# Kernel optimization log

Hardware: AMD Instinct MI355X
Metric: run time of the kernel (lower is better)

The kernel has to match this reference:

```python
import jax, jax.numpy as jnp
import numpy as np
from jax import lax

DIM = 256
HEADS = 8
SR = 4
EPS = 1e-5
SCALE = (DIM // HEADS) ** -0.5


def _dwconv(x, wgt, stride, pad):
    # x: (B,C,H,W), wgt: (C,1,kh,kw) depthwise
    return lax.conv_general_dilated(
        x, wgt, (stride, stride), [(pad, pad), (pad, pad)],
        feature_group_count=x.shape[1],
        dimension_numbers=("NCHW", "OIHW", "NCHW"))


def _bn(x, g, b, m, v):
    # eval-mode batchnorm folded to per-channel scale/shift
    s = g / jnp.sqrt(v + EPS)
    return x * s[:, None, None] + (b - m * s)[:, None, None]


def setup_inputs() -> dict:
    key = jax.random.key(0)
    ks = jax.random.split(key, 16)
    b, h, w = 8, 64, 64
    c = DIM
    n = h * w

    def rn(k, shape, s=0.05):
        return jax.random.normal(k, shape, jnp.float32) * s

    return dict(
        x=jax.random.normal(ks[0], (b, n, c), jnp.float32),
        h=h, w=w,
        Wq=rn(ks[1], (c, c)), bq=rn(ks[2], (c,)),
        Wkv=rn(ks[3], (2 * c, c)), bkv=rn(ks[4], (2 * c,)),
        sr_w1=rn(ks[5], (c, 1, SR + 3, SR + 3), 0.1),
        bn1_gamma=1.0 + rn(ks[6], (c,)), bn1_beta=rn(ks[7], (c,)),
        bn1_mean=rn(ks[8], (c,)), bn1_var=jnp.abs(1.0 + rn(ks[9], (c,))),
        sr_w2=1.0 + rn(ks[10], (c,), 0.2),  # 1x1 depthwise conv == per-channel scale
        bn2_gamma=1.0 + rn(ks[11], (c,)), bn2_beta=rn(ks[12], (c,)),
        bn2_mean=rn(ks[13], (c,)), bn2_var=jnp.abs(1.0 + rn(ks[14], (c,))),
        local_w=rn(ks[15], (c, 1, 3, 3), 0.1),
        local_b=jnp.zeros((c,), jnp.float32),
    )


def reference(x, h, w, Wq, bq, Wkv, bkv, sr_w1, bn1_gamma, bn1_beta, bn1_mean,
              bn1_var, sr_w2, bn2_gamma, bn2_beta, bn2_mean, bn2_var,
              local_w, local_b):
    b, n, c = x.shape
    hd = c // HEADS
    xi = x.transpose(0, 2, 1).reshape(b, c, h, w)  # (b,c,h,w)

    # q projection (1x1 conv == channel matmul)
    q = jnp.einsum("bchw,dc->bdhw", xi, Wq) + bq[None, :, None, None]
    q = q.reshape(b, HEADS, hd, n).transpose(0, 1, 3, 2)  # (b,H,n,hd)

    # spatial reduction: dwconv7 s4 + BN + GELU + dw1x1 + BN
    kv = _dwconv(xi, sr_w1, SR, (SR + 3) // 2)
    kv = _bn(kv, bn1_gamma, bn1_beta, bn1_mean, bn1_var)
    kv = jax.nn.gelu(kv, approximate=False)
    kv = kv * sr_w2[None, :, None, None]
    kv = _bn(kv, bn2_gamma, bn2_beta, bn2_mean, bn2_var)

    # residual local depthwise 3x3 conv
    kv = _dwconv(kv, local_w, 1, 1) + local_b[None, :, None, None] + kv

    # kv projection and split
    kvp = jnp.einsum("bchw,dc->bdhw", kv, Wkv) + bkv[None, :, None, None]
    k_, v_ = jnp.split(kvp, 2, axis=1)
    m = k_.shape[2] * k_.shape[3]
    k_ = k_.reshape(b, HEADS, hd, m)                       # (b,H,hd,m)
    v_ = v_.reshape(b, HEADS, hd, m).transpose(0, 1, 3, 2)  # (b,H,m,hd)

    attn = jax.nn.softmax(jnp.einsum("bhnd,bhdm->bhnm", q, k_) * SCALE, axis=-1)
    out = jnp.einsum("bhnm,bhmd->bhnd", attn, v_)           # (b,H,n,hd)
    out = out.transpose(0, 1, 3, 2).reshape(b, c, n).transpose(0, 2, 1)
    return out
```

## Files before the change

### kernel.cpp

```cpp
#include <hip/hip_runtime.h>
#include <math.h>

typedef __bf16 bf16;
typedef bf16 bf16x4 __attribute__((ext_vector_type(4)));
typedef bf16 bf16x8 __attribute__((ext_vector_type(8)));
typedef float f32x4 __attribute__((ext_vector_type(4)));

static_assert(sizeof(bf16x8) == 16, "bf16x8 must be 16B");

#define QSCALE (0.17677669529663687f * 1.4426950408889634f)

__device__ __forceinline__ f32x4 mfma16(bf16x8 a, bf16x8 b, f32x4 c) {
  return __builtin_amdgcn_mfma_f32_16x16x32_bf16(a, b, c, 0, 0, 0);
}

__global__ __launch_bounds__(256) void k_cvt(
    const float* __restrict__ Wq, const float* __restrict__ Wkv,
    const float* __restrict__ w7, bf16* __restrict__ Wqb,
    bf16* __restrict__ Wkvb, float* __restrict__ w7t) {
  const int tid = threadIdx.x;
  const int blk = blockIdx.x;
  if (blk < 96) {
    const float* src;
    bf16* dst;
    if (blk < 32) {
      const int idx = blk * 256 + tid;
      src = Wq + (size_t)idx * 8;
      dst = Wqb + (size_t)idx * 8;
    } else {
      const int idx = (blk - 32) * 256 + tid;
      src = Wkv + (size_t)idx * 8;
      dst = Wkvb + (size_t)idx * 8;
    }
    const float4 a = ((const float4*)src)[0];
    const float4 b = ((const float4*)src)[1];
    bf16x8 r;
    r[0] = (bf16)a.x; r[1] = (bf16)a.y; r[2] = (bf16)a.z; r[3] = (bf16)a.w;
    r[4] = (bf16)b.x; r[5] = (bf16)b.y; r[6] = (bf16)b.z; r[7] = (bf16)b.w;
    *(bf16x8*)dst = r;
  } else {
    const int c = tid;
    #pragma unroll
    for (int tap = 0; tap < 49; tap++)
      w7t[tap * 256 + c] = w7[c * 49 + tap];
  }
}

__global__ __launch_bounds__(256, 2) void k_sr(
    const float* __restrict__ x, const float* __restrict__ w7t,
    const float* __restrict__ g1, const float* __restrict__ b1,
    const float* __restrict__ m1, const float* __restrict__ v1,
    const float* __restrict__ sw2,
    const float* __restrict__ g2, const float* __restrict__ b2,
    const float* __restrict__ m2, const float* __restrict__ v2,
    bf16* __restrict__ kv1) {
  __shared__ float part[4][256];
  const int tid = threadIdx.x;
  const int team = tid >> 6, g = tid & 63;
  const int c0 = g * 4;
  const int blk = blockIdx.x;
  const int b = blk & 7, m = blk >> 3;
  const int oy = m >> 4, ox = m & 15;

  float4 xv[13], wv[13];
  float msk[13];
  #pragma unroll
  for (int j = 0; j < 13; j++) {
    const int tap = team + j * 4;
    const int ky = tap / 7, kx = tap - ky * 7;
    const int iy = oy * 4 - 3 + ky, ix = ox * 4 - 3 + kx;
    msk[j] = (tap < 49 && iy >= 0 && iy < 64 && ix >= 0 && ix < 64) ? 1.f : 0.f;
    const int iyc = iy < 0 ? 0 : (iy > 63 ? 63 : iy);
    const int ixc = ix < 0 ? 0 : (ix > 63 ? 63 : ix);
    const int tc = tap > 48 ? 48 : tap;
    xv[j] = *(const float4*)(x + ((size_t)b * 4096 + iyc * 64 + ixc) * 256 + c0);
    wv[j] = *(const float4*)(w7t + tc * 256 + c0);
  }
  float a0 = 0.f, a1 = 0.f, a2 = 0.f, a3 = 0.f;
  #pragma unroll
  for (int j = 0; j < 13; j++) {
    a0 += xv[j].x * wv[j].x * msk[j];
    a1 += xv[j].y * wv[j].y * msk[j];
    a2 += xv[j].z * wv[j].z * msk[j];
    a3 += xv[j].w * wv[j].w * msk[j];
  }
  *(f32x4*)&part[team][c0] = (f32x4){a0, a1, a2, a3};
  __syncthreads();
  const int c = tid;
  float y = part[0][c] + part[1][c] + part[2][c] + part[3][c];
  float s = g1[c] / sqrtf(v1[c] + 1e-5f);
  y = y * s + (b1[c] - m1[c] * s);
  y = 0.5f * y * (1.f + erff(y * 0.70710678118654752f));
  y *= sw2[c];
  s = g2[c] / sqrtf(v2[c] + 1e-5f);
  y = y * s + (b2[c] - m2[c] * s);
  kv1[((size_t)b * 256 + m) * 256 + c] = (bf16)y;
}

__global__ __launch_bounds__(256) void k_localkv(
    const bf16* __restrict__ kv1, const float* __restrict__ w3,
    const float* __restrict__ lb, const bf16* __restrict__ Wkvb,
    const float* __restrict__ bkv, bf16* __restrict__ k_a,
    bf16* __restrict__ v_b) {
  __shared__ bf16 halo[3][10][256];
  __shared__ float rows[8][256];
  const int c = threadIdx.x;
  const int mt = blockIdx.x;
  const int part = blockIdx.y;
  const int b = blockIdx.z;
  const int oy = mt >> 1, o0 = (mt & 1) * 8;

  #pragma unroll
  for (int p = 0; p < 30; p++) {
    const int dy = p / 10, xi = p - dy * 10;
    const int iy = oy - 1 + dy, ix = o0 - 1 + xi;
    const bool ok = (iy >= 0 && iy < 16 && ix >= 0 && ix < 16);
    const int iyc = ok ? iy : 0, ixc = ok ? ix : 0;
    const bf16 v = kv1[((size_t)b * 256 + iyc * 16 + ixc) * 256 + c];
    halo[dy][xi][c] = ok ? v : (bf16)0.f;
  }
  float w3f[9];
  #pragma unroll
  for (int t = 0; t < 9; t++) w3f[t] = w3[c * 9 + t];
  const float lbf = lb[c];
  __syncthreads();

  #pragma unroll
  for (int r = 0; r < 8; r++) {
    float acc = lbf + (float)halo[1][r + 1][c];
    #pragma unroll
    for (int ky = 0; ky < 3; ky++)
      #pragma unroll
      for (int kx = 0; kx < 3; kx++)
        acc += (float)halo[ky][r + kx][c] * w3f[ky * 3 + kx];
    rows[r][c] = acc;
  }
  __syncthreads();

  const int tid = c;
  const size_t wrow = (size_t)tid + (part ? 256 : 0);
  float accs[8] = {0};
  for (int oc = 0; oc < 32; oc++) {
    const bf16x8 w0 = *(const bf16x8*)(Wkvb + wrow * 256 + oc * 8);
    float wf0[8];
    #pragma unroll
    for (int j = 0; j < 8; j++) wf0[j] = (float)w0[j];
    #pragma unroll
    for (int r = 0; r < 8; r++) {
      const float4* rp = (const float4*)&rows[r][oc * 8];
      const float4 ra = rp[0], rb = rp[1];
      const float rv[8] = {ra.x, ra.y, ra.z, ra.w, rb.x, rb.y, rb.z, rb.w};
      #pragma unroll
      for (int j = 0; j < 8; j++) accs[r] += wf0[j] * rv[j];
    }
  }
  const float bias = bkv[wrow];
  const int h = tid >> 5, d = tid & 31;
  if (part == 0) {
    #pragma unroll
    for (int r = 0; r < 8; r++) {
      const int m = (oy * 16 + o0) + r;
      k_a[(((size_t)b * 8 + h) * 256 + m) * 32 + d] = (bf16)(accs[r] + bias);
    }
  } else {
    #pragma unroll
    for (int r = 0; r < 8; r++) {
      const int m = (oy * 16 + o0) + r;
      v_b[(((size_t)b * 8 + h) * 32 + d) * 256 + m] = (bf16)(accs[r] + bias);
    }
  }
}

__global__ __launch_bounds__(256) void k_qproj(
    const float* __restrict__ x, const bf16* __restrict__ Wqb,
    const float* __restrict__ bq, bf16* __restrict__ q_ws) {
  __shared__ bf16 xs[32 * 264];
  const int tid = threadIdx.x, wv = tid >> 6, lane = tid & 63;
  const int qd = lane >> 4, l15 = lane & 15;
  const size_t rowbase = (size_t)blockIdx.x * 32;

  #pragma unroll
  for (int it = 0; it < 4; it++) {
    const int idx = it * 256 + tid;
    const int lr = idx >> 5, pos = idx & 31;
    const float* src = x + (rowbase + lr) * 256 + pos * 8;
    const float4 a = ((const float4*)src)[0];
    const float4 b = ((const float4*)src)[1];
    bf16x8 r;
    r[0] = (bf16)a.x; r[1] = (bf16)a.y; r[2] = (bf16)a.z; r[3] = (bf16)a.w;
    r[4] = (bf16)b.x; r[5] = (bf16)b.y; r[6] = (bf16)b.z; r[7] = (bf16)b.w;
    *(bf16x8*)(xs + lr * 264 + pos * 8) = r;
  }
  __syncthreads();

  f32x4 acc0[4], acc1[4];
  #pragma unroll
  for (int dt = 0; dt < 4; dt++) {
    acc0[dt] = (f32x4){0.f, 0.f, 0.f, 0.f};
    acc1[dt] = (f32x4){0.f, 0.f, 0.f, 0.f};
  }
  #pragma unroll 2
  for (int kc = 0; kc < 8; kc++) {
    const bf16x8 a0 = *(const bf16x8*)(xs + l15 * 264 + kc * 32 + qd * 8);
    const bf16x8 a1 = *(const bf16x8*)(xs + (16 + l15) * 264 + kc * 32 + qd * 8);
    #pragma unroll
    for (int dt = 0; dt < 4; dt++) {
      const int d = wv * 64 + dt * 16 + l15;
      const bf16x8 bb = *(const bf16x8*)(Wqb + (size_t)d * 256 + kc * 32 + qd * 8);
      acc0[dt] = mfma16(a0, bb, acc0[dt]);
      acc1[dt] = mfma16(a1, bb, acc1[dt]);
    }
  }
  #pragma unroll
  for (int dt = 0; dt < 4; dt++) {
    const int d = wv * 64 + dt * 16 + l15;
    const float bias = bq[d];
    const int h = d >> 5, dl = d & 31;
    #pragma unroll
    for (int r = 0; r < 4; r++) {
      const size_t row0 = rowbase + qd * 4 + r;
      const size_t row1 = rowbase + 16 + qd * 4 + r;
      q_ws[(((row0 >> 12) * 8 + h) * 4096 + (row0 & 4095)) * 32 + dl] =
          (bf16)((acc0[dt][r] + bias) * QSCALE);
      q_ws[(((row1 >> 12) * 8 + h) * 4096 + (row1 & 4095)) * 32 + dl] =
          (bf16)((acc1[dt][r] + bias) * QSCALE);
    }
  }
}

__global__ __launch_bounds__(256) void k_attn(
    const bf16* __restrict__ q_ws, const bf16* __restrict__ k_a,
    const bf16* __restrict__ v_b, float* __restrict__ out) {
  __shared__ float comb[2][36][64];
  const int tid = threadIdx.x;
  const int wv = tid >> 6, lane = tid & 63;
  const int pair = wv >> 1, half = wv & 1;
  const int qd = lane >> 4, l15 = lane & 15;
  const int b = blockIdx.z, h = blockIdx.y;
  const int bh = b * 8 + h;
  const int n_base = blockIdx.x * 128 + pair * 64;

  const bf16* qb = q_ws + ((size_t)bh * 4096 + n_base) * 32;
  bf16x8 qf[4];
  #pragma unroll
  for (int qi = 0; qi < 4; qi++)
    qf[qi] = *(const bf16x8*)(qb + (size_t)(qi * 16 + l15) * 32 + qd * 8);

  const bf16* kb = k_a + ((size_t)bh * 256 + half * 128) * 32;
  const bf16* vb = v_b + (size_t)bh * 32 * 256 + half * 128;

  f32x4 acc[4][2];
  float lr[4] = {0.f, 0.f, 0.f, 0.f};
  #pragma unroll
  for (int qi = 0; qi < 4; qi++) {
    acc[qi][0] = (f32x4){0.f, 0.f, 0.f, 0.f};
    acc[qi][1] = (f32x4){0.f, 0.f, 0.f, 0.f};
  }
  const int kperm = 8 * (l15 >> 2) + (l15 & 3);

  bf16x8 ka0 = *(const bf16x8*)(kb + (size_t)kperm * 32 + qd * 8);
  bf16x8 ka1 = *(const bf16x8*)(kb + (size_t)(kperm + 4) * 32 + qd * 8);
  bf16x8 va0 = *(const bf16x8*)(vb + (size_t)l15 * 256 + qd * 8);
  bf16x8 va1 = *(const bf16x8*)(vb + (size_t)(16 + l15) * 256 + qd * 8);

  for (int ch = 0; ch < 4; ch++) {
    const int cn = (ch < 3 ? ch + 1 : 3) * 32;
    const bf16x8 nk0 = *(const bf16x8*)(kb + (size_t)(cn + kperm) * 32 + qd * 8);
    const bf16x8 nk1 = *(const bf16x8*)(kb + (size_t)(cn + kperm + 4) * 32 + qd * 8);
    const bf16x8 nv0 = *(const bf16x8*)(vb + (size_t)l15 * 256 + cn + qd * 8);
    const bf16x8 nv1 = *(const bf16x8*)(vb + (size_t)(16 + l15) * 256 + cn + qd * 8);
    const f32x4 z = (f32x4){0.f, 0.f, 0.f, 0.f};
    #pragma unroll
    for (int qi = 0; qi < 4; qi++) {
      f32x4 s0 = mfma16(ka0, qf[qi], z);
      f32x4 s1 = mfma16(ka1, qf[qi], z);
      float p[8], ls = 0.f;
      #pragma unroll
      for (int j = 0; j < 4; j++) {
        p[j] = __builtin_amdgcn_exp2f(fminf(s0[j], 80.f));
        p[4 + j] = __builtin_amdgcn_exp2f(fminf(s1[j], 80.f));
      }
      #pragma unroll
      for (int j = 0; j < 8; j++) ls += p[j];
      lr[qi] += ls;
      bf16x8 pb;
      #pragma unroll
      for (int j = 0; j < 8; j++) pb[j] = (bf16)p[j];
      acc[qi][0] = mfma16(va0, pb, acc[qi][0]);
      acc[qi][1] = mfma16(va1, pb, acc[qi][1]);
    }
    ka0 = nk0; ka1 = nk1; va0 = nv0; va1 = nv1;
  }

  if (half == 1) {
    #pragma unroll
    for (int qi = 0; qi < 4; qi++)
      #pragma unroll
      for (int t = 0; t < 2; t++)
        #pragma unroll
        for (int j = 0; j < 4; j++)
          comb[pair][qi * 8 + t * 4 + j][lane] = acc[qi][t][j];
    #pragma unroll
    for (int qi = 0; qi < 4; qi++) comb[pair][32 + qi][lane] = lr[qi];
  }
  __syncthreads();
  if (half == 0) {
    #pragma unroll
    for (int qi = 0; qi < 4; qi++) {
      #pragma unroll
      for (int t = 0; t < 2; t++)
        #pragma unroll
        for (int j = 0; j < 4; j++)
          acc[qi][t][j] += comb[pair][qi * 8 + t * 4 + j][lane];
      lr[qi] += comb[pair][32 + qi][lane];
    }
    #pragma unroll
    for (int qi = 0; qi < 4; qi++) {
      float l = lr[qi];
      l += __shfl_xor(l, 16, 64);
      l += __shfl_xor(l, 32, 64);
      const float inv = 1.f / l;
      const int nn = n_base + qi * 16 + l15;
      float* ob = out + (size_t)(b * 4096 + nn) * 256 + h * 32;
      #pragma unroll
      for (int t = 0; t < 2; t++) {
        *(float4*)(ob + t * 16 + qd * 4) =
            (float4){acc[qi][t][0] * inv, acc[qi][t][1] * inv,
                     acc[qi][t][2] * inv, acc[qi][t][3] * inv};
      }
    }
  }
}

extern "C" void kernel_launch(void* const* d_in, const int* in_sizes, int n_in,
                              void* d_out, int out_size, void* d_ws, size_t ws_size,
                              hipStream_t stream) {
  const float* x      = (const float*)d_in[0];
  const float* Wq     = (const float*)d_in[3];
  const float* bq     = (const float*)d_in[4];
  const float* Wkv    = (const float*)d_in[5];
  const float* bkv    = (const float*)d_in[6];
  const float* sr_w1  = (const float*)d_in[7];
  const float* bn1_g  = (const float*)d_in[8];
  const float* bn1_b  = (const float*)d_in[9];
  const float* bn1_m  = (const float*)d_in[10];
  const float* bn1_v  = (const float*)d_in[11];
  const float* sw2    = (const float*)d_in[12];
  const float* bn2_g  = (const float*)d_in[13];
  const float* bn2_b  = (const float*)d_in[14];
  const float* bn2_m  = (const float*)d_in[15];
  const float* bn2_v  = (const float*)d_in[16];
  const float* lw     = (const float*)d_in[17];
  const float* lb     = (const float*)d_in[18];

  const int B = in_sizes[0] / (4096 * 256);

  bf16* Wqb  = (bf16*)d_ws;
  bf16* Wkvb = Wqb + 65536;
  float* w7t = (float*)(Wkvb + 131072);
  bf16* kv1  = (bf16*)(w7t + 12544);
  bf16* k_a  = kv1 + (size_t)B * 256 * 256;
  bf16* v_b  = k_a + (size_t)B * 8 * 256 * 32;
  bf16* q_ws = v_b + (size_t)B * 8 * 32 * 256;

  k_cvt<<<dim3(97), 256, 0, stream>>>(Wq, Wkv, sr_w1, Wqb, Wkvb, w7t);
  k_sr<<<dim3(256 * B), 256, 0, stream>>>(x, w7t, bn1_g, bn1_b, bn1_m, bn1_v,
                                          sw2, bn2_g, bn2_b, bn2_m, bn2_v, kv1);
  k_localkv<<<dim3(32, 2, B), 256, 0, stream>>>(kv1, lw, lb, Wkvb, bkv, k_a, v_b);
  k_qproj<<<dim3(B * 128), 256, 0, stream>>>(x, Wqb, bq, q_ws);
  k_attn<<<dim3(32, 8, B), 256, 0, stream>>>(q_ws, k_a, v_b, (float*)d_out);
}
```

Before: 184.1 us.

## Merge all five stages into one persistent cooperative kernel with grid syncs

Replaces the five separate launches (weight convert, spatial reduction, local conv + kv projection, q projection, attention) with a single cooperative kernel of 512 blocks. The blocks loop over the same work items and separate the stages with grid.sync. The q projection now runs in the same phase as the spatial reduction. The intent is to remove launch gaps and per-kernel tail effects. The cost is grid-wide barriers, a fixed grid size that caps parallelism in the local-kv phase, and a fallback to the old launches if the cooperative launch fails.

```diff
diff --git a/kernel.cpp b/kernel.cpp
--- a/kernel.cpp
+++ b/kernel.cpp
@@ -1,5 +1,8 @@
 #include <hip/hip_runtime.h>
+#include <hip/hip_cooperative_groups.h>
 #include <math.h>
+
+namespace cg = cooperative_groups;
 
 typedef __bf16 bf16;
 typedef bf16 bf16x4 __attribute__((ext_vector_type(4)));
@@ -12,6 +15,336 @@
 
 __device__ __forceinline__ f32x4 mfma16(bf16x8 a, bf16x8 b, f32x4 c) {
   return __builtin_amdgcn_mfma_f32_16x16x32_bf16(a, b, c, 0, 0, 0);
+}
+
+__global__ __launch_bounds__(256, 2) void k_mega(
+    const float* __restrict__ x, const float* __restrict__ Wq,
+    const float* __restrict__ Wkv, const float* __restrict__ w7,
+    const float* __restrict__ bq, const float* __restrict__ bkv,
+    const float* __restrict__ g1, const float* __restrict__ b1,
+    const float* __restrict__ m1, const float* __restrict__ v1,
+    const float* __restrict__ sw2, const float* __restrict__ g2,
+    const float* __restrict__ b2, const float* __restrict__ m2,
+    const float* __restrict__ v2, const float* __restrict__ lw,
+    const float* __restrict__ lb, bf16* __restrict__ Wqb,
+    bf16* __restrict__ Wkvb, float* __restrict__ w7t, bf16* __restrict__ kv1,
+    bf16* __restrict__ k_a, bf16* __restrict__ v_b, bf16* __restrict__ q_ws,
+    float* __restrict__ out, int B) {
+  cg::grid_group grid = cg::this_grid();
+  __shared__ __align__(16) unsigned char smem[23552];
+  const int tid = threadIdx.x;
+  const int bi = blockIdx.x;
+  const int NB = gridDim.x;
+
+  if (bi < 97) {
+    const int blk = bi;
+    if (blk < 96) {
+      const float* src;
+      bf16* dst;
+      if (blk < 32) {
+        const int idx = blk * 256 + tid;
+        src = Wq + (size_t)idx * 8;
+        dst = Wqb + (size_t)idx * 8;
+      } else {
+        const int idx = (blk - 32) * 256 + tid;
+        src = Wkv + (size_t)idx * 8;
+        dst = Wkvb + (size_t)idx * 8;
+      }
+      const float4 a = ((const float4*)src)[0];
+      const float4 b = ((const float4*)src)[1];
+      bf16x8 r;
+      r[0] = (bf16)a.x; r[1] = (bf16)a.y; r[2] = (bf16)a.z; r[3] = (bf16)a.w;
+      r[4] = (bf16)b.x; r[5] = (bf16)b.y; r[6] = (bf16)b.z; r[7] = (bf16)b.w;
+      *(bf16x8*)dst = r;
+    } else {
+      const int c = tid;
+      #pragma unroll
+      for (int tap = 0; tap < 49; tap++)
+        w7t[tap * 256 + c] = w7[c * 49 + tap];
+    }
+  }
+  __threadfence();
+  grid.sync();
+
+  for (int it = bi; it < B * 384; it += NB) {
+    if (it < B * 128) {
+      bf16* xs = (bf16*)smem;
+      const int wv = tid >> 6, lane = tid & 63;
+      const int qd = lane >> 4, l15 = lane & 15;
+      const size_t rowbase = (size_t)it * 32;
+
+      #pragma unroll
+      for (int t = 0; t < 4; t++) {
+        const int idx = t * 256 + tid;
+        const int lr = idx >> 5, pos = idx & 31;
+        const float* src = x + (rowbase + lr) * 256 + pos * 8;
+        const float4 a = ((const float4*)src)[0];
+        const float4 b = ((const float4*)src)[1];
+        bf16x8 r;
+        r[0] = (bf16)a.x; r[1] = (bf16)a.y; r[2] = (bf16)a.z; r[3] = (bf16)a.w;
+        r[4] = (bf16)b.x; r[5] = (bf16)b.y; r[6] = (bf16)b.z; r[7] = (bf16)b.w;
+        *(bf16x8*)(xs + lr * 264 + pos * 8) = r;
+      }
+      __syncthreads();
+
+      f32x4 acc0[4], acc1[4];
+      #pragma unroll
+      for (int dt = 0; dt < 4; dt++) {
+        acc0[dt] = (f32x4){0.f, 0.f, 0.f, 0.f};
+        acc1[dt] = (f32x4){0.f, 0.f, 0.f, 0.f};
+      }
+      #pragma unroll 2
+      for (int kc = 0; kc < 8; kc++) {
+        const bf16x8 a0 = *(const bf16x8*)(xs + l15 * 264 + kc * 32 + qd * 8);
+        const bf16x8 a1 =
+            *(const bf16x8*)(xs + (16 + l15) * 264 + kc * 32 + qd * 8);
+        #pragma unroll
+        for (int dt = 0; dt < 4; dt++) {
+          const int d = wv * 64 + dt * 16 + l15;
+          const bf16x8 bb =
+              *(const bf16x8*)(Wqb + (size_t)d * 256 + kc * 32 + qd * 8);
+          acc0[dt] = mfma16(a0, bb, acc0[dt]);
+          acc1[dt] = mfma16(a1, bb, acc1[dt]);
+        }
+      }
+      #pragma unroll
+      for (int dt = 0; dt < 4; dt++) {
+        const int d = wv * 64 + dt * 16 + l15;
+        const float bias = bq[d];
+        const int h = d >> 5, dl = d & 31;
+        #pragma unroll
+        for (int r = 0; r < 4; r++) {
+          const size_t row0 = rowbase + qd * 4 + r;
+          const size_t row1 = rowbase + 16 + qd * 4 + r;
+          q_ws[(((row0 >> 12) * 8 + h) * 4096 + (row0 & 4095)) * 32 + dl] =
+              (bf16)((acc0[dt][r] + bias) * QSCALE);
+          q_ws[(((row1 >> 12) * 8 + h) * 4096 + (row1 & 4095)) * 32 + dl] =
+              (bf16)((acc1[dt][r] + bias) * QSCALE);
+        }
+      }
+    } else {
+      float (*part)[256] = (float (*)[256])smem;
+      const int team = tid >> 6, g = tid & 63;
+      const int c0 = g * 4;
+      const int blk = it - B * 128;
+      const int b = blk & 7, m = blk >> 3;
+      const int oy = m >> 4, ox = m & 15;
+
+      float4 xv[13], wv13[13];
+      float msk[13];
+      #pragma unroll
+      for (int j = 0; j < 13; j++) {
+        const int tap = team + j * 4;
+        const int ky = tap / 7, kx = tap - ky * 7;
+        const int iy = oy * 4 - 3 + ky, ix = ox * 4 - 3 + kx;
+        msk[j] =
+            (tap < 49 && iy >= 0 && iy < 64 && ix >= 0 && ix < 64) ? 1.f : 0.f;
+        const int iyc = iy < 0 ? 0 : (iy > 63 ? 63 : iy);
+        const int ixc = ix < 0 ? 0 : (ix > 63 ? 63 : ix);
+        const int tc = tap > 48 ? 48 : tap;
+        xv[j] =
+            *(const float4*)(x + ((size_t)b * 4096 + iyc * 64 + ixc) * 256 + c0);
+        wv13[j] = *(const float4*)(w7t + tc * 256 + c0);
+      }
+      float a0 = 0.f, a1 = 0.f, a2 = 0.f, a3 = 0.f;
+      #pragma unroll
+      for (int j = 0; j < 13; j++) {
+        a0 += xv[j].x * wv13[j].x * msk[j];
+        a1 += xv[j].y * wv13[j].y * msk[j];
+        a2 += xv[j].z * wv13[j].z * msk[j];
+        a3 += xv[j].w * wv13[j].w * msk[j];
+      }
+      *(f32x4*)&part[team][c0] = (f32x4){a0, a1, a2, a3};
+      __syncthreads();
+      const int c = tid;
+      float y = part[0][c] + part[1][c] + part[2][c] + part[3][c];
+      float s = g1[c] / sqrtf(v1[c] + 1e-5f);
+      y = y * s + (b1[c] - m1[c] * s);
+      y = 0.5f * y * (1.f + erff(y * 0.70710678118654752f));
+      y *= sw2[c];
+      s = g2[c] / sqrtf(v2[c] + 1e-5f);
+      y = y * s + (b2[c] - m2[c] * s);
+      kv1[((size_t)b * 256 + m) * 256 + c] = (bf16)y;
+    }
+    __syncthreads();
+  }
+  __threadfence();
+  grid.sync();
+
+  if (bi < B * 64) {
+    bf16 (*halo)[10][256] = (bf16 (*)[10][256])smem;
+    float (*rows)[256] = (float (*)[256])(smem + 15360);
+    const int c = tid;
+    const int mt = bi & 31;
+    const int partk = (bi >> 5) & 1;
+    const int b = bi >> 6;
+    const int oy = mt >> 1, o0 = (mt & 1) * 8;
+
+    #pragma unroll
+    for (int p = 0; p < 30; p++) {
+      const int dy = p / 10, xi = p - dy * 10;
+      const int iy = oy - 1 + dy, ix = o0 - 1 + xi;
+      const bool ok = (iy >= 0 && iy < 16 && ix >= 0 && ix < 16);
+      const int iyc = ok ? iy : 0, ixc = ok ? ix : 0;
+      const bf16 v = kv1[((size_t)b * 256 + iyc * 16 + ixc) * 256 + c];
+      halo[dy][xi][c] = ok ? v : (bf16)0.f;
+    }
+    float w3f[9];
+    #pragma unroll
+    for (int t = 0; t < 9; t++) w3f[t] = lw[c * 9 + t];
+    const float lbf = lb[c];
+    __syncthreads();
+
+    #pragma unroll
+    for (int r = 0; r < 8; r++) {
+      float acc = lbf + (float)halo[1][r + 1][c];
+      #pragma unroll
+      for (int ky = 0; ky < 3; ky++)
+        #pragma unroll
+        for (int kx = 0; kx < 3; kx++)
+          acc += (float)halo[ky][r + kx][c] * w3f[ky * 3 + kx];
+      rows[r][c] = acc;
+    }
+    __syncthreads();
+
+    const size_t wrow = (size_t)tid + (partk ? 256 : 0);
+    float accs[8] = {0};
+    for (int oc = 0; oc < 32; oc++) {
+      const bf16x8 w0 = *(const bf16x8*)(Wkvb + wrow * 256 + oc * 8);
+      float wf0[8];
+      #pragma unroll
+      for (int j = 0; j < 8; j++) wf0[j] = (float)w0[j];
+      #pragma unroll
+      for (int r = 0; r < 8; r++) {
+        const float4* rp = (const float4*)&rows[r][oc * 8];
+        const float4 ra = rp[0], rb = rp[1];
+        const float rv[8] = {ra.x, ra.y, ra.z, ra.w, rb.x, rb.y, rb.z, rb.w};
+        #pragma unroll
+        for (int j = 0; j < 8; j++) accs[r] += wf0[j] * rv[j];
+      }
+    }
+    const float bias = bkv[wrow];
+    const int h = tid >> 5, d = tid & 31;
+    if (partk == 0) {
+      #pragma unroll
+      for (int r = 0; r < 8; r++) {
+        const int m = (oy * 16 + o0) + r;
+        k_a[(((size_t)b * 8 + h) * 256 + m) * 32 + d] = (bf16)(accs[r] + bias);
+      }
+    } else {
+      #pragma unroll
+      for (int r = 0; r < 8; r++) {
+        const int m = (oy * 16 + o0) + r;
+        v_b[(((size_t)b * 8 + h) * 32 + d) * 256 + m] = (bf16)(accs[r] + bias);
+      }
+    }
+  }
+  __threadfence();
+  grid.sync();
+
+  for (int it = bi; it < B * 256; it += NB) {
+    float (*comb)[36][64] = (float (*)[36][64])smem;
+    const int wv = tid >> 6, lane = tid & 63;
+    const int pair = wv >> 1, half = wv & 1;
+    const int qd = lane >> 4, l15 = lane & 15;
+    const int xb = it & 31, h = (it >> 5) & 7, b = it >> 8;
+    const int bh = b * 8 + h;
+    const int n_base = xb * 128 + pair * 64;
+
+    const bf16* qb = q_ws + ((size_t)bh * 4096 + n_base) * 32;
+    bf16x8 qf[4];
+    #pragma unroll
+    for (int qi = 0; qi < 4; qi++)
+      qf[qi] = *(const bf16x8*)(qb + (size_t)(qi * 16 + l15) * 32 + qd * 8);
+
+    const bf16* kb = k_a + ((size_t)bh * 256 + half * 128) * 32;
+    const bf16* vb = v_b + (size_t)bh * 32 * 256 + half * 128;
+
+    f32x4 acc[4][2];
+    float lr[4] = {0.f, 0.f, 0.f, 0.f};
+    #pragma unroll
+    for (int qi = 0; qi < 4; qi++) {
+      acc[qi][0] = (f32x4){0.f, 0.f, 0.f, 0.f};
+      acc[qi][1] = (f32x4){0.f, 0.f, 0.f, 0.f};
+    }
+    const int kperm = 8 * (l15 >> 2) + (l15 & 3);
+
+    bf16x8 ka0 = *(const bf16x8*)(kb + (size_t)kperm * 32 + qd * 8);
+    bf16x8 ka1 = *(const bf16x8*)(kb + (size_t)(kperm + 4) * 32 + qd * 8);
+    bf16x8 va0 = *(const bf16x8*)(vb + (size_t)l15 * 256 + qd * 8);
+    bf16x8 va1 = *(const bf16x8*)(vb + (size_t)(16 + l15) * 256 + qd * 8);
+
+    for (int ch = 0; ch < 4; ch++) {
+      const int cn = (ch < 3 ? ch + 1 : 3) * 32;
+      const bf16x8 nk0 = *(const bf16x8*)(kb + (size_t)(cn + kperm) * 32 + qd * 8);
+      const bf16x8 nk1 =
+          *(const bf16x8*)(kb + (size_t)(cn + kperm + 4) * 32 + qd * 8);
+      const bf16x8 nv0 = *(const bf16x8*)(vb + (size_t)l15 * 256 + cn + qd * 8);
+      const bf16x8 nv1 =
+          *(const bf16x8*)(vb + (size_t)(16 + l15) * 256 + cn + qd * 8);
+      const f32x4 z = (f32x4){0.f, 0.f, 0.f, 0.f};
+      #pragma unroll
+      for (int qi = 0; qi < 4; qi++) {
+        f32x4 s0 = mfma16(ka0, qf[qi], z);
+        f32x4 s1 = mfma16(ka1, qf[qi], z);
+        float p[8], ls = 0.f;
+        #pragma unroll
+        for (int j = 0; j < 4; j++) {
+          p[j] = __builtin_amdgcn_exp2f(fminf(s0[j], 80.f));
+          p[4 + j] = __builtin_amdgcn_exp2f(fminf(s1[j], 80.f));
+        }
+        #pragma unroll
+        for (int j = 0; j < 8; j++) ls += p[j];
+        lr[qi] += ls;
+        bf16x8 pb;
+        #pragma unroll
+        for (int j = 0; j < 8; j++) pb[j] = (bf16)p[j];
+        acc[qi][0] = mfma16(va0, pb, acc[qi][0]);
+        acc[qi][1] = mfma16(va1, pb, acc[qi][1]);
+      }
+      ka0 = nk0; ka1 = nk1; va0 = nv0; va1 = nv1;
+    }
+
+    if (half == 1) {
+      #pragma unroll
+      for (int qi = 0; qi < 4; qi++)
+        #pragma unroll
+        for (int t = 0; t < 2; t++)
+          #pragma unroll
+          for (int j = 0; j < 4; j++)
+            comb[pair][qi * 8 + t * 4 + j][lane] = acc[qi][t][j];
+      #pragma unroll
+      for (int qi = 0; qi < 4; qi++) comb[pair][32 + qi][lane] = lr[qi];
+    }
+    __syncthreads();
+    if (half == 0) {
+      #pragma unroll
+      for (int qi = 0; qi < 4; qi++) {
+        #pragma unroll
+        for (int t = 0; t < 2; t++)
+          #pragma unroll
+          for (int j = 0; j < 4; j++)
+            acc[qi][t][j] += comb[pair][qi * 8 + t * 4 + j][lane];
+        lr[qi] += comb[pair][32 + qi][lane];
+      }
+      #pragma unroll
+      for (int qi = 0; qi < 4; qi++) {
+        float l = lr[qi];
+        l += __shfl_xor(l, 16, 64);
+        l += __shfl_xor(l, 32, 64);
+        const float inv = 1.f / l;
+        const int nn = n_base + qi * 16 + l15;
+        float* ob = out + (size_t)(b * 4096 + nn) * 256 + h * 32;
+        #pragma unroll
+        for (int t = 0; t < 2; t++) {
+          *(float4*)(ob + t * 16 + qd * 4) =
+              (float4){acc[qi][t][0] * inv, acc[qi][t][1] * inv,
+                       acc[qi][t][2] * inv, acc[qi][t][3] * inv};
+        }
+      }
+    }
+    __syncthreads();
+  }
 }
 
 __global__ __launch_bounds__(256) void k_cvt(
@@ -353,7 +686,7 @@
   const float* lw     = (const float*)d_in[17];
   const float* lb     = (const float*)d_in[18];
 
-  const int B = in_sizes[0] / (4096 * 256);
+  int B = in_sizes[0] / (4096 * 256);
 
   bf16* Wqb  = (bf16*)d_ws;
   bf16* Wkvb = Wqb + 65536;
@@ -362,11 +695,23 @@
   bf16* k_a  = kv1 + (size_t)B * 256 * 256;
   bf16* v_b  = k_a + (size_t)B * 8 * 256 * 32;
   bf16* q_ws = v_b + (size_t)B * 8 * 32 * 256;
-
-  k_cvt<<<dim3(97), 256, 0, stream>>>(Wq, Wkv, sr_w1, Wqb, Wkvb, w7t);
-  k_sr<<<dim3(256 * B), 256, 0, stream>>>(x, w7t, bn1_g, bn1_b, bn1_m, bn1_v,
-                                          sw2, bn2_g, bn2_b, bn2_m, bn2_v, kv1);
-  k_localkv<<<dim3(32, 2, B), 256, 0, stream>>>(kv1, lw, lb, Wkvb, bkv, k_a, v_b);
-  k_qproj<<<dim3(B * 128), 256, 0, stream>>>(x, Wqb, bq, q_ws);
-  k_attn<<<dim3(32, 8, B), 256, 0, stream>>>(q_ws, k_a, v_b, (float*)d_out);
+  float* outp = (float*)d_out;
+
+  void* args[] = {&x,     &Wq,    &Wkv,   &sr_w1, &bq,    &bkv,  &bn1_g,
+                  &bn1_b, &bn1_m, &bn1_v, &sw2,   &bn2_g, &bn2_b, &bn2_m,
+                  &bn2_v, &lw,    &lb,    &Wqb,   &Wkvb,  &w7t,  &kv1,
+                  &k_a,   &v_b,   &q_ws,  &outp,  &B};
+  hipError_t err = hipLaunchCooperativeKernel((void*)k_mega, dim3(512),
+                                              dim3(256), args, 0, stream);
+  if (err != hipSuccess) {
+    (void)hipGetLastError();
+    k_cvt<<<dim3(97), 256, 0, stream>>>(Wq, Wkv, sr_w1, Wqb, Wkvb, w7t);
+    k_sr<<<dim3(256 * B), 256, 0, stream>>>(x, w7t, bn1_g, bn1_b, bn1_m, bn1_v,
+                                            sw2, bn2_g, bn2_b, bn2_m, bn2_v,
+                                            kv1);
+    k_localkv<<<dim3(32, 2, B), 256, 0, stream>>>(kv1, lw, lb, Wkvb, bkv, k_a,
+                                                  v_b);
+    k_qproj<<<dim3(B * 128), 256, 0, stream>>>(x, Wqb, bq, q_ws);
+    k_attn<<<dim3(32, 8, B), 256, 0, stream>>>(q_ws, k_a, v_b, outp);
+  }
 }
```

Result: slower. 534.7 us (+190.4%).
